# Performance work log

Measured on AMD Instinct MI355X. Metric: run time of the kernel, lower is better.

The kernel has to match this reference:

```python
import jax, jax.numpy as jnp
import numpy as np

D_MODEL = 1024
N_HEADS = 16
HEAD_DIM = D_MODEL // N_HEADS  # 64
SEQ = 2048
BATCH = 2


def setup_inputs() -> dict:
    key = jax.random.key(0)
    ks = jax.random.split(key, 12)
    s = 1.0 / np.sqrt(D_MODEL)
    return {
        "query": jax.random.normal(ks[0], (SEQ, BATCH, D_MODEL), jnp.float32),
        "key": jax.random.normal(ks[1], (SEQ, BATCH, D_MODEL), jnp.float32),
        "value": jax.random.normal(ks[2], (SEQ, BATCH, D_MODEL), jnp.float32),
        "Wq": jax.random.normal(ks[3], (D_MODEL, D_MODEL), jnp.float32) * s,
        "bq": jax.random.normal(ks[4], (D_MODEL,), jnp.float32) * s,
        "Wk": jax.random.normal(ks[5], (D_MODEL, D_MODEL), jnp.float32) * s,
        "bk": jax.random.normal(ks[6], (D_MODEL,), jnp.float32) * s,
        "Wv": jax.random.normal(ks[7], (D_MODEL, D_MODEL), jnp.float32) * s,
        "bv": jax.random.normal(ks[8], (D_MODEL,), jnp.float32) * s,
        "Wo": jax.random.normal(ks[9], (D_MODEL, D_MODEL), jnp.float32) * s,
        "bo": jax.random.normal(ks[10], (D_MODEL,), jnp.float32) * s,
    }


def _rope_tables(seq_len):
    # theta_i = 1 / 10000^(2i/head_dim), i in [0, head_dim//2)
    theta = 1.0 / (10000.0 ** (2.0 * jnp.arange(HEAD_DIM // 2, dtype=jnp.float32) / HEAD_DIM))
    pos = jnp.arange(seq_len, dtype=jnp.float32)[:, None, None, None] * theta  # [S,1,1,hd/2]
    return jnp.sin(pos), jnp.cos(pos)


def _apply_rope(t, sin, cos):
    # t: [S, B, H, hd]; NOTE faithful to source: t2 = q1*sin - q2*cos (minus)
    h = HEAD_DIM // 2
    q1, q2 = t[..., :h], t[..., h:]
    return jnp.concatenate([q1 * cos - q2 * sin, q1 * sin - q2 * cos], axis=-1)


def reference(query, key, value, Wq, bq, Wk, bk, Wv, bv, Wo, bo):
    S, B, _ = query.shape
    q = (query @ Wq.T + bq).reshape(S, B, N_HEADS, HEAD_DIM)
    k = (key @ Wk.T + bk).reshape(S, B, N_HEADS, HEAD_DIM)
    v = (value @ Wv.T + bv).reshape(S, B, N_HEADS, HEAD_DIM)
    sin, cos = _rope_tables(S)
    q = _apply_rope(q, sin, cos)
    k = _apply_rope(k, sin, cos)
    # [S,B,H,d] -> [B,H,S,d]
    q = q.transpose(1, 2, 0, 3)
    k = k.transpose(1, 2, 0, 3)
    v = v.transpose(1, 2, 0, 3)
    scale = 1.0 / jnp.sqrt(jnp.float32(HEAD_DIM))
    scores = jnp.einsum("bhqd,bhkd->bhqk", q, k) * scale
    attn = jax.nn.softmax(scores, axis=-1)
    out = jnp.einsum("bhqk,bhkd->bhqd", attn, v)  # [B,H,S,d]
    out = out.transpose(2, 0, 1, 3).reshape(S, B, D_MODEL)
    return out @ Wo.T + bo
```

## Files before the change

### kernel.cpp

```cpp
#include <hip/hip_runtime.h>
#include <hip/hip_bf16.h>

#define DMODEL 1024
#define NHEADS 16
#define HDIM   64
#define SEQ    2048
#define BATCH  2
#define MROWS  (SEQ*BATCH)

typedef unsigned int u32;
typedef unsigned short u16;
typedef __attribute__((ext_vector_type(8))) short bfrag;
typedef __attribute__((ext_vector_type(4))) float f32x4;
typedef __attribute__((ext_vector_type(16))) float f32x16;
typedef union { u32 u[4]; bfrag f; } fragu;

#define LOG2E 1.44269504088896341f

__device__ __forceinline__ u32 f2bf(float x) {
    unsigned u = __float_as_uint(x);
    return (u + 0x7fffu + ((u >> 16) & 1u)) >> 16;
}
__device__ __forceinline__ float bf2f(u32 h) {
    return __uint_as_float(h << 16);
}
__device__ __forceinline__ u32 pk2bf(float a, float b) {
    __hip_bfloat162 t = __float22bfloat162_rn(make_float2(a, b));
    u32 r;
    __builtin_memcpy(&r, &t, 4);
    return r;
}
__device__ __forceinline__ float fexp2(float x) {
#if __has_builtin(__builtin_amdgcn_exp2f)
    return __builtin_amdgcn_exp2f(x);
#else
    return exp2f(x);
#endif
}
__device__ __forceinline__ u32 pkhi(u32 u0, u32 u1) {
#if __has_builtin(__builtin_amdgcn_perm)
    return __builtin_amdgcn_perm(u1, u0, 0x07060302u);
#else
    return (u0 >> 16) | (u1 & 0xffff0000u);
#endif
}

__device__ __forceinline__ void gld16(const void* g, void* l) {
    __builtin_amdgcn_global_load_lds(
        (const __attribute__((address_space(1))) unsigned int*)g,
        (__attribute__((address_space(3))) unsigned int*)l, 16, 0, 0);
}


__global__ __launch_bounds__(256) void prep_kernel(
    const float* __restrict__ Wq, const float* __restrict__ Wk,
    const float* __restrict__ Wv, const float* __restrict__ Wo,
    u16* __restrict__ wqb, u16* __restrict__ wkb, u16* __restrict__ wvb,
    u16* __restrict__ wob, float2* __restrict__ tab)
{
    const int y = blockIdx.y;
    if (y == 3) {
        if (blockIdx.x >= 256) return;
        const int e = blockIdx.x * 256 + threadIdx.x;
        const int s = e >> 5, i = e & 31;
        const double th = exp(-(double)i * (9.210340371976184 / 32.0));
        double sn, cs;
        sincos((double)s * th, &sn, &cs);
        tab[e] = make_float2((float)sn, (float)cs);
        return;
    }
    const float* src = (y == 0) ? Wq : (y == 1) ? Wk : (y == 2) ? Wv : Wo;
    u16* dst = (y == 0) ? wqb : (y == 1) ? wkb : (y == 2) ? wvb : wob;
    const int lane = threadIdx.x & 63;
    const int wv   = threadIdx.x >> 6;
    const int g8   = lane >> 3;
    const int l8   = lane & 7;
    for (int r = 0; r < 2; ++r) {
        const size_t kb = (size_t)blockIdx.x * 8 + (size_t)r * 4 + wv;
        const float4 x4 = *(const float4*)(src + kb * 256 + lane * 4);
        __align__(8) u16 hb[4];
        __align__(8) u16 lb[4];
        const float xs[4] = {x4.x, x4.y, x4.z, x4.w};
        #pragma unroll
        for (int i = 0; i < 4; ++i) {
            const u32 h = f2bf(xs[i]);
            hb[i] = (u16)h;
            lb[i] = (u16)f2bf(xs[i] - bf2f(h));
        }
        u16* o = dst + kb * 512 + g8 * 64 + l8 * 4;
        *(uint2*)o        = *(const uint2*)hb;
        *(uint2*)(o + 32) = *(const uint2*)lb;
    }
}

__global__ __launch_bounds__(256) void qkv_gemm_kernel(
    const float* __restrict__ query, const float* __restrict__ key,
    const float* __restrict__ value,
    const u16* __restrict__ Wqb, const u16* __restrict__ Wkb,
    const u16* __restrict__ Wvb,
    const float* __restrict__ bq, const float* __restrict__ bk,
    const float* __restrict__ bv, const float2* __restrict__ tab,
    u16* __restrict__ Qh, u16* __restrict__ Ql,
    u16* __restrict__ Kh, u16* __restrict__ Kl,
    u16* __restrict__ VTh)
{
    __shared__ u16 smem16[32768];
    u16* sA = smem16;
    u16* sB = smem16 + 16384;

    const int z  = blockIdx.z;
    const float* Af   = (z == 0) ? query : (z == 1) ? key : value;
    const u16* Wb     = (z == 0) ? Wqb : (z == 1) ? Wkb : Wvb;
    const float* bias = (z == 0) ? bq : (z == 1) ? bk : bv;
    u16* Oh = (z == 0) ? Qh : (z == 1) ? Kh : VTh;
    u16* Ol = (z == 0) ? Ql : (z == 1) ? Kl : nullptr;
    const float rope_scale = (z == 0) ? 0.125f * LOG2E : 1.0f;
    const int mode = (z == 2) ? 1 : 0;

    const int tid   = threadIdx.x;
    const int w     = tid >> 6;
    const int lane  = tid & 63;
    const int lrow  = lane & 15;
    const int lquad = lane >> 4;

    const int id   = blockIdx.x + 16 * blockIdx.y;
    const int xcd  = id & 7;
    const int jj   = id >> 3;
    const int nblk = jj & 7;
    const int mblk = (xcd << 2) | (jj >> 3);
    const int n0   = nblk * 128;
    const int m0   = mblk * 128;

    const int srow8 = lane >> 3;
    const int sch   = (lane & 7) ^ srow8;

    const int l8r = lane >> 3;
    const int l8c = lane & 7;
    const int cA  = l8c >> 1;
    const int hA  = (l8c & 1) * 4;

    int aoffh[2], aoffl[2], boffh[8], boffl[8];
    #pragma unroll
    for (int mi = 0; mi < 2; ++mi) {
        const int ra = w * 32 + mi * 16 + lrow;
        aoffh[mi] = ra * 64 + ((lquad ^ (ra & 7)) << 3);
        aoffl[mi] = ra * 64 + (((lquad + 4) ^ (ra & 7)) << 3);
    }
    #pragma unroll
    for (int ni = 0; ni < 8; ++ni) {
        const int rb = ni * 16 + lrow;
        boffh[ni] = rb * 64 + ((lquad ^ (rb & 7)) << 3);
        boffl[ni] = rb * 64 + (((lquad + 4) ^ (rb & 7)) << 3);
    }

    f32x4 acc[2][8] = {};

    auto stageB = [&](int t) {
        const int h = t & 1;
        #pragma unroll
        for (int i = 0; i < 4; ++i) {
            const int slab = w * 4 + i;
            const int row  = slab * 8 + srow8;
            gld16(Wb + (size_t)(n0 + row) * 2048 + t * 64 + sch * 8,
                  sB + h * 8192 + slab * 512);
        }
    };
    auto loadA = [&](int t, float4* va) {
        #pragma unroll
        for (int i = 0; i < 4; ++i) {
            const int r = w * 32 + i * 8 + l8r;
            va[i] = ((const float4*)Af)[(size_t)(m0 + r) * 256 + t * 8 + l8c];
        }
    };
    auto writeA = [&](int t, const float4* va) {
        const int h = t & 1;
        #pragma unroll
        for (int i = 0; i < 4; ++i) {
            const int r = w * 32 + i * 8 + l8r;
            const u32 u0 = __float_as_uint(va[i].x);
            const u32 u1 = __float_as_uint(va[i].y);
            const u32 u2 = __float_as_uint(va[i].z);
            const u32 u3 = __float_as_uint(va[i].w);
            uint2 hv, lv;
            hv.x = pkhi(u0, u1);
            hv.y = pkhi(u2, u3);
            const float r0 = va[i].x - __uint_as_float(u0 & 0xffff0000u);
            const float r1 = va[i].y - __uint_as_float(u1 & 0xffff0000u);
            const float r2 = va[i].z - __uint_as_float(u2 & 0xffff0000u);
            const float r3 = va[i].w - __uint_as_float(u3 & 0xffff0000u);
            lv.x = pk2bf(r0, r1);
            lv.y = pk2bf(r2, r3);
            u16* base = sA + h * 8192 + r * 64;
            *(uint2*)(base + ((cA ^ (r & 7)) << 3) + hA)       = hv;
            *(uint2*)(base + (((cA + 4) ^ (r & 7)) << 3) + hA) = lv;
        }
    };

    {
        float4 va[4];
        stageB(0);
        loadA(0, va);
        writeA(0, va);
    }
    for (int t = 0; t < 32; ++t) {
        __syncthreads();
        float4 va[4];
        if (t < 31) {
            stageB(t + 1);
            loadA(t + 1, va);
        }
        const int h = t & 1;
        const u16* sAh_ = sA + h * 8192;
        const u16* sBh_ = sB + h * 8192;

        bfrag ah[2], al[2], bh[8], bl[8];
        #pragma unroll
        for (int mi = 0; mi < 2; ++mi) {
            ah[mi] = *(const bfrag*)&sAh_[aoffh[mi]];
            al[mi] = *(const bfrag*)&sAh_[aoffl[mi]];
        }
        #pragma unroll
        for (int ni = 0; ni < 8; ++ni) {
            bh[ni] = *(const bfrag*)&sBh_[boffh[ni]];
            bl[ni] = *(const bfrag*)&sBh_[boffl[ni]];
        }

        #pragma unroll
        for (int mi = 0; mi < 2; ++mi)
            #pragma unroll
            for (int ni = 0; ni < 8; ++ni) {
                acc[mi][ni] = __builtin_amdgcn_mfma_f32_16x16x32_bf16(ah[mi], bh[ni], acc[mi][ni], 0, 0, 0);
                acc[mi][ni] = __builtin_amdgcn_mfma_f32_16x16x32_bf16(ah[mi], bl[ni], acc[mi][ni], 0, 0, 0);
                acc[mi][ni] = __builtin_amdgcn_mfma_f32_16x16x32_bf16(al[mi], bh[ni], acc[mi][ni], 0, 0, 0);
            }

        if (t < 31) writeA(t + 1, va);
    }

    float bn[8];
    #pragma unroll
    for (int ni = 0; ni < 8; ++ni) bn[ni] = bias[n0 + ni * 16 + lrow];

    if (mode == 0) {
        #pragma unroll
        for (int mi = 0; mi < 2; ++mi)
            #pragma unroll
            for (int r = 0; r < 4; ++r) {
                const int mrow = w * 32 + mi * 16 + lquad * 4 + r;
                const int m  = m0 + mrow;
                const int bb = m & 1;
                const int sg = m >> 1;
                #pragma unroll
                for (int hh = 0; hh < 2; ++hh) {
                    const int head = nblk * 2 + hh;
                    const size_t ob = (((size_t)(bb * NHEADS + head) * SEQ) + sg) * HDIM;
                    #pragma unroll
                    for (int ni = 0; ni < 2; ++ni) {
                        const int i = ni * 16 + lrow;
                        const float2 sc = tab[(size_t)sg * 32 + i];
                        const float x1 = acc[mi][hh * 4 + ni][r]     + bn[hh * 4 + ni];
                        const float x2 = acc[mi][hh * 4 + ni + 2][r] + bn[hh * 4 + ni + 2];
                        const float o1 = (x1 * sc.y - x2 * sc.x) * rope_scale;
                        const float o2 = (x1 * sc.x - x2 * sc.y) * rope_scale;
                        const u32 h1 = f2bf(o1);
                        const u32 h2 = f2bf(o2);
                        Oh[ob + i]      = (u16)h1;  Ol[ob + i]      = (u16)f2bf(o1 - bf2f(h1));
                        Oh[ob + i + 32] = (u16)h2;  Ol[ob + i + 32] = (u16)f2bf(o2 - bf2f(h2));
                    }
                }
            }
        return;
    }
    __syncthreads();
    u32* vb = (u32*)smem16;
    for (int p = 0; p < 2; ++p) {
        if (p) __syncthreads();
        #pragma unroll
        for (int mi = 0; mi < 2; ++mi)
            #pragma unroll
            for (int r = 0; r < 4; ++r) {
                const int mrow = w * 32 + mi * 16 + lquad * 4 + r;
                const int bb = mrow & 1;
                const int sl = mrow >> 1;
                if (bb == p) {
                    #pragma unroll
                    for (int ni = 0; ni < 8; ++ni) {
                        const int d = ni * 16 + lrow;
                        vb[d * 65 + sl] = f2bf(acc[mi][ni][r] + bn[ni]);
                    }
                }
            }
        __syncthreads();
        #pragma unroll
        for (int rep = 0; rep < 4; ++rep) {
            const int c  = rep * 256 + tid;
            const int dc = c >> 3;
            const int s8 = c & 7;
            __align__(8) u16 hb[8];
            #pragma unroll
            for (int j = 0; j < 8; ++j)
                hb[j] = (u16)vb[dc * 65 + s8 * 8 + j];
            const int head = nblk * 2 + (dc >> 6);
            const int dd   = dc & 63;
            const size_t orow = ((size_t)(p * NHEADS + head) * HDIM + dd) * SEQ + (m0 >> 1);
            const int blk16 = (s8 >> 1) * 16;
            const int off   = (s8 & 1) * 4;
            *(uint2*)&Oh[orow + blk16 + off]     = *(const uint2*)&hb[0];
            *(uint2*)&Oh[orow + blk16 + 8 + off] = *(const uint2*)&hb[4];
        }
    }
}

template <int NI>
__device__ __forceinline__ void gemm_body(
    int id,
    const u16* __restrict__ Ab, const u16* __restrict__ Wb,
    const float* __restrict__ bias, float* __restrict__ Of,
    u16* smem16)
{
    u16* sA = smem16;
    u16* sB = smem16 + 16384;

    const int tid   = threadIdx.x;
    const int w     = tid >> 6;
    const int lane  = tid & 63;
    const int lrow  = lane & 15;
    const int lquad = lane >> 4;

    const int NBLK = 1024 / (NI * 16);
    const int xcd  = id & 7;
    const int jj   = id >> 3;
    const int nblk = jj & (NBLK - 1);
    const int mblk = (xcd << 2) | (jj / NBLK);
    const int n0   = nblk * NI * 16;
    const int m0   = mblk * 128;

    const int srow8 = lane >> 3;
    const int sch   = (lane & 7) ^ srow8;

    int aoffh[2], aoffl[2], boffh[NI], boffl[NI];
    #pragma unroll
    for (int mi = 0; mi < 2; ++mi) {
        const int ra = w * 32 + mi * 16 + lrow;
        aoffh[mi] = ra * 64 + ((lquad ^ (ra & 7)) << 3);
        aoffl[mi] = ra * 64 + (((lquad + 4) ^ (ra & 7)) << 3);
    }
    #pragma unroll
    for (int ni = 0; ni < NI; ++ni) {
        const int rb = ni * 16 + lrow;
        boffh[ni] = rb * 64 + ((lquad ^ (rb & 7)) << 3);
        boffl[ni] = rb * 64 + (((lquad + 4) ^ (rb & 7)) << 3);
    }

    f32x4 acc[2][NI] = {};

    auto stage = [&](int t) {
        const int h = t & 1;
        #pragma unroll
        for (int i = 0; i < 4; ++i) {
            const int slab = w * 4 + i;
            const int row  = slab * 8 + srow8;
            gld16(Ab + (size_t)(m0 + row) * 2048 + t * 64 + sch * 8,
                  sA + h * 8192 + slab * 512);
        }
        #pragma unroll
        for (int i = 0; i < NI / 2; ++i) {
            const int slab = w * (NI / 2) + i;
            const int row  = slab * 8 + srow8;
            gld16(Wb + (size_t)(n0 + row) * 2048 + t * 64 + sch * 8,
                  sB + h * (NI * 1024) + slab * 512);
        }
    };

    stage(0);
    for (int t = 0; t < 32; ++t) {
        __syncthreads();
        if (t < 31) stage(t + 1);
        const int h = t & 1;
        const u16* sAh_ = sA + h * 8192;
        const u16* sBh_ = sB + h * (NI * 1024);

        bfrag ah[2], al[2], bh[NI], bl[NI];
        #pragma unroll
        for (int mi = 0; mi < 2; ++mi) {
            ah[mi] = *(const bfrag*)&sAh_[aoffh[mi]];
            al[mi] = *(const bfrag*)&sAh_[aoffl[mi]];
        }
        #pragma unroll
        for (int ni = 0; ni < NI; ++ni) {
            bh[ni] = *(const bfrag*)&sBh_[boffh[ni]];
            bl[ni] = *(const bfrag*)&sBh_[boffl[ni]];
        }

        #pragma unroll
        for (int mi = 0; mi < 2; ++mi)
            #pragma unroll
            for (int ni = 0; ni < NI; ++ni) {
                acc[mi][ni] = __builtin_amdgcn_mfma_f32_16x16x32_bf16(ah[mi], bh[ni], acc[mi][ni], 0, 0, 0);
                acc[mi][ni] = __builtin_amdgcn_mfma_f32_16x16x32_bf16(ah[mi], bl[ni], acc[mi][ni], 0, 0, 0);
                acc[mi][ni] = __builtin_amdgcn_mfma_f32_16x16x32_bf16(al[mi], bh[ni], acc[mi][ni], 0, 0, 0);
            }
    }

    float bn[NI];
    #pragma unroll
    for (int ni = 0; ni < NI; ++ni) bn[ni] = bias[n0 + ni * 16 + lrow];

    #pragma unroll
    for (int mi = 0; mi < 2; ++mi)
        #pragma unroll
        for (int r = 0; r < 4; ++r) {
            const int m = m0 + w * 32 + mi * 16 + lquad * 4 + r;
            #pragma unroll
            for (int ni = 0; ni < NI; ++ni)
                Of[(size_t)m * 1024 + n0 + ni * 16 + lrow] = acc[mi][ni][r] + bn[ni];
        }
}

__global__ __launch_bounds__(256) void out_gemm_kernel(
    const u16* __restrict__ Ab, const u16* __restrict__ Wb,
    const float* __restrict__ bias, float* __restrict__ Of)
{
    __shared__ u16 smem16[24576];
    const int id = blockIdx.x + 16 * blockIdx.y;
    gemm_body<4>(id, Ab, Wb, bias, Of, smem16);
}

__global__ __launch_bounds__(256) void attn_mfma_kernel(
    const u16* __restrict__ Qh, const u16* __restrict__ Ql,
    const u16* __restrict__ Kh, const u16* __restrict__ Kl,
    const u16* __restrict__ Vh,
    u16* __restrict__ AOb)
{
    __shared__ u16 sKh[8192], sKl[8192];
    __shared__ u16 sVh[8192];

    const int tid  = threadIdx.x;
    const int w    = tid >> 6;
    const int lane = tid & 63;
    const int l31  = lane & 31;
    const int g    = lane >> 5;

    const int id = blockIdx.x + 16 * blockIdx.y;
    const int jj = id >> 3;
    const int bh = ((id & 7) << 2) | (jj >> 4);
    const int qt = jj & 15;

    const size_t qg = ((size_t)bh * SEQ + qt * 128 + w * 32 + l31) * HDIM + g * 8;
    bfrag qfh[4], qfl[4];
    #pragma unroll
    for (int ks = 0; ks < 4; ++ks) {
        qfh[ks] = *(const bfrag*)&Qh[qg + ks * 16];
        qfl[ks] = *(const bfrag*)&Ql[qg + ks * 16];
    }

    const int srow   = lane >> 3;
    const int schunk = (lane & 7) ^ srow;
    const u16* gsrc = nullptr; u16* lbase = nullptr; size_t istep = 0, ktstep = 0;
    if (w == 0) {
        gsrc = Kh + ((size_t)bh * SEQ + srow) * HDIM + schunk * 8;
        istep = 8 * 64; ktstep = 64 * 64; lbase = sKh;
    } else if (w == 1) {
        gsrc = Kl + ((size_t)bh * SEQ + srow) * HDIM + schunk * 8;
        istep = 8 * 64; ktstep = 64 * 64; lbase = sKl;
    } else if (w == 2) {
        gsrc = Vh + ((size_t)bh * HDIM + srow) * SEQ + schunk * 8;
        istep = 8 * SEQ; ktstep = 64; lbase = sVh;
    }

    int koff[2][4];
    #pragma unroll
    for (int a = 0; a < 2; ++a) {
        const int row = a * 32 + l31;
        #pragma unroll
        for (int c = 0; c < 4; ++c)
            koff[a][c] = row * 64 + (((c * 2 + g) ^ (row & 7)) << 3);
    }

    f32x16 accO[2] = {};
    float l_loc = 0.0f;

    auto stage = [&](int kt) {
        if (w < 3) {
            const u16* gp = gsrc + (size_t)kt * ktstep;
            u16* dst = lbase + (kt & 1) * 4096;
            #pragma unroll
            for (int i = 0; i < 8; ++i)
                gld16(gp + (size_t)i * istep, dst + i * 512);
        }
    };

    stage(0);
    for (int kt = 0; kt < SEQ / 64; ++kt) {
        __syncthreads();
        if (kt < SEQ / 64 - 1) stage(kt + 1);
        const int po = (kt & 1) * 4096;

        f32x16 accS[2] = {};
        #pragma unroll
        for (int kg = 0; kg < 2; ++kg)
            #pragma unroll
            for (int ks = 0; ks < 4; ++ks) {
                const bfrag kh_ = *(const bfrag*)&sKh[po + koff[kg][ks]];
                const bfrag kl_ = *(const bfrag*)&sKl[po + koff[kg][ks]];
                accS[kg] = __builtin_amdgcn_mfma_f32_32x32x16_bf16(kh_, qfh[ks], accS[kg], 0, 0, 0);
                accS[kg] = __builtin_amdgcn_mfma_f32_32x32x16_bf16(kh_, qfl[ks], accS[kg], 0, 0, 0);
                accS[kg] = __builtin_amdgcn_mfma_f32_32x32x16_bf16(kl_, qfh[ks], accS[kg], 0, 0, 0);
            }

        float pv[2][16];
        #pragma unroll
        for (int kg = 0; kg < 2; ++kg)
            #pragma unroll
            for (int r = 0; r < 16; ++r) {
                const float p = fexp2(accS[kg][r]);
                pv[kg][r] = p;
                l_loc += p;
            }

        #pragma unroll
        for (int kp = 0; kp < 4; ++kp) {
            const int kg = kp >> 1;
            const int t8 = (kp & 1) * 8;
            fragu ph;
            #pragma unroll
            for (int j2 = 0; j2 < 4; ++j2)
                ph.u[j2] = pk2bf(pv[kg][t8 + 2 * j2], pv[kg][t8 + 2 * j2 + 1]);
            #pragma unroll
            for (int dt = 0; dt < 2; ++dt) {
                const bfrag vh = *(const bfrag*)&sVh[po + koff[dt][kp]];
                accO[dt] = __builtin_amdgcn_mfma_f32_32x32x16_bf16(vh, ph.f, accO[dt], 0, 0, 0);
            }
        }
    }

    const float inv = 1.0f / (l_loc + __shfl_xor(l_loc, 32));

    const int b = bh >> 4;
    const int h = bh & 15;
    const int sg = qt * 128 + w * 32 + l31;
    const int rm = sg * BATCH + b;
    #pragma unroll
    for (int dt = 0; dt < 2; ++dt)
        #pragma unroll
        for (int rq = 0; rq < 4; ++rq) {
            const int j0 = 8 * rq + 4 * g;
            const int t  = h * 2 + dt;
            __align__(8) u16 hb[4];
            __align__(8) u16 lb[4];
            #pragma unroll
            for (int i2 = 0; i2 < 4; ++i2) {
                const float v = accO[dt][rq * 4 + i2] * inv;
                const u32 hh = f2bf(v);
                hb[i2] = (u16)hh;
                lb[i2] = (u16)f2bf(v - bf2f(hh));
            }
            u16* o = AOb + (size_t)rm * 2048 + t * 64 + j0;
            *(uint2*)o        = *(const uint2*)hb;
            *(uint2*)(o + 32) = *(const uint2*)lb;
        }
}

extern "C" void kernel_launch(void* const* d_in, const int* in_sizes, int n_in,
                              void* d_out, int out_size, void* d_ws, size_t ws_size,
                              hipStream_t stream)
{
    const float* query = (const float*)d_in[0];
    const float* key   = (const float*)d_in[1];
    const float* value = (const float*)d_in[2];
    const float* Wq    = (const float*)d_in[3];
    const float* bq    = (const float*)d_in[4];
    const float* Wk    = (const float*)d_in[5];
    const float* bk    = (const float*)d_in[6];
    const float* Wv    = (const float*)d_in[7];
    const float* bv    = (const float*)d_in[8];
    const float* Wo    = (const float*)d_in[9];
    const float* bo    = (const float*)d_in[10];
    float* out = (float*)d_out;

    char* wsb = (char*)d_ws;
    const size_t MB = 1024 * 1024;
    u16* Wqb = (u16*)(wsb + 0 * MB);
    u16* Wkb = (u16*)(wsb + 4 * MB);
    u16* Wvb = (u16*)(wsb + 8 * MB);
    float2* tab = (float2*)(wsb + 12 * MB);
    u16* Qh  = (u16*)(wsb + 16 * MB); u16* Ql  = (u16*)(wsb + 24 * MB);
    u16* Kh  = (u16*)(wsb + 32 * MB); u16* Kl  = (u16*)(wsb + 40 * MB);
    u16* VTh = (u16*)(wsb + 48 * MB);
    u16* Wob = (u16*)(wsb + 56 * MB);
    u16* AOb = (u16*)(wsb + 0 * MB);

    prep_kernel<<<dim3(512, 5), 256, 0, stream>>>(
        Wq, Wk, Wv, Wo, Wqb, Wkb, Wvb, Wob, tab);
    qkv_gemm_kernel<<<dim3(16, 16, 3), 256, 0, stream>>>(
        query, key, value,
        Wqb, Wkb, Wvb, bq, bk, bv, tab, Qh, Ql, Kh, Kl, VTh);
    attn_mfma_kernel<<<dim3(16, 32), 256, 0, stream>>>(
        Qh, Ql, Kh, Kl, VTh, AOb);
    out_gemm_kernel<<<dim3(16, 32), 256, 0, stream>>>(AOb, Wob, bo, out);
}
```

Baseline: 316.0 us.

## Stage fp32 A tiles via direct global-to-LDS loads and split to bf16 after LDS read

```diff
diff --git a/kernel.cpp b/kernel.cpp
--- a/kernel.cpp
+++ b/kernel.cpp
@@ -105,8 +105,8 @@
     u16* __restrict__ VTh)
 {
     __shared__ u16 smem16[32768];
-    u16* sA = smem16;
-    u16* sB = smem16 + 16384;
+    float* sAf = (float*)smem16;
+    u16*   sB  = smem16 + 16384;
 
     const int z  = blockIdx.z;
     const float* Af   = (z == 0) ? query : (z == 1) ? key : value;
@@ -134,18 +134,14 @@
     const int srow8 = lane >> 3;
     const int sch   = (lane & 7) ^ srow8;
 
-    const int l8r = lane >> 3;
-    const int l8c = lane & 7;
-    const int cA  = l8c >> 1;
-    const int hA  = (l8c & 1) * 4;
-
-    int aoffh[2], aoffl[2], boffh[8], boffl[8];
+    int aoff0[2], aoff1[2];
     #pragma unroll
     for (int mi = 0; mi < 2; ++mi) {
         const int ra = w * 32 + mi * 16 + lrow;
-        aoffh[mi] = ra * 64 + ((lquad ^ (ra & 7)) << 3);
-        aoffl[mi] = ra * 64 + (((lquad + 4) ^ (ra & 7)) << 3);
-    }
+        aoff0[mi] = ra * 32 + (((2 * lquad)     ^ (ra & 7)) << 2);
+        aoff1[mi] = ra * 32 + (((2 * lquad + 1) ^ (ra & 7)) << 2);
+    }
+    int boffh[8], boffl[8];
     #pragma unroll
     for (int ni = 0; ni < 8; ++ni) {
         const int rb = ni * 16 + lrow;
@@ -155,69 +151,52 @@
 
     f32x4 acc[2][8] = {};
 
-    auto stageB = [&](int t) {
+    auto stage = [&](int t) {
         const int h = t & 1;
         #pragma unroll
         for (int i = 0; i < 4; ++i) {
             const int slab = w * 4 + i;
             const int row  = slab * 8 + srow8;
+            gld16(Af + (size_t)(m0 + row) * 1024 + t * 32 + sch * 4,
+                  sAf + h * 4096 + slab * 256);
             gld16(Wb + (size_t)(n0 + row) * 2048 + t * 64 + sch * 8,
                   sB + h * 8192 + slab * 512);
         }
     };
-    auto loadA = [&](int t, float4* va) {
-        #pragma unroll
-        for (int i = 0; i < 4; ++i) {
-            const int r = w * 32 + i * 8 + l8r;
-            va[i] = ((const float4*)Af)[(size_t)(m0 + r) * 256 + t * 8 + l8c];
-        }
+
+    auto cvtAB = [&](const f32x4 a, const f32x4 b, bfrag& hi8, bfrag& lo8) {
+        const u32 u0 = __float_as_uint(a[0]), u1 = __float_as_uint(a[1]);
+        const u32 u2 = __float_as_uint(a[2]), u3 = __float_as_uint(a[3]);
+        const u32 u4 = __float_as_uint(b[0]), u5 = __float_as_uint(b[1]);
+        const u32 u6 = __float_as_uint(b[2]), u7 = __float_as_uint(b[3]);
+        fragu fh, fl;
+        fh.u[0] = pkhi(u0, u1); fh.u[1] = pkhi(u2, u3);
+        fh.u[2] = pkhi(u4, u5); fh.u[3] = pkhi(u6, u7);
+        fl.u[0] = pk2bf(a[0] - __uint_as_float(u0 & 0xffff0000u),
+                        a[1] - __uint_as_float(u1 & 0xffff0000u));
+        fl.u[1] = pk2bf(a[2] - __uint_as_float(u2 & 0xffff0000u),
+                        a[3] - __uint_as_float(u3 & 0xffff0000u));
+        fl.u[2] = pk2bf(b[0] - __uint_as_float(u4 & 0xffff0000u),
+                        b[1] - __uint_as_float(u5 & 0xffff0000u));
+        fl.u[3] = pk2bf(b[2] - __uint_as_float(u6 & 0xffff0000u),
+                        b[3] - __uint_as_float(u7 & 0xffff0000u));
+        hi8 = fh.f; lo8 = fl.f;
     };
-    auto writeA = [&](int t, const float4* va) {
-        const int h = t & 1;
-        #pragma unroll
-        for (int i = 0; i < 4; ++i) {
-            const int r = w * 32 + i * 8 + l8r;
-            const u32 u0 = __float_as_uint(va[i].x);
-            const u32 u1 = __float_as_uint(va[i].y);
-            const u32 u2 = __float_as_uint(va[i].z);
-            const u32 u3 = __float_as_uint(va[i].w);
-            uint2 hv, lv;
-            hv.x = pkhi(u0, u1);
-            hv.y = pkhi(u2, u3);
-            const float r0 = va[i].x - __uint_as_float(u0 & 0xffff0000u);
-            const float r1 = va[i].y - __uint_as_float(u1 & 0xffff0000u);
-            const float r2 = va[i].z - __uint_as_float(u2 & 0xffff0000u);
-            const float r3 = va[i].w - __uint_as_float(u3 & 0xffff0000u);
-            lv.x = pk2bf(r0, r1);
-            lv.y = pk2bf(r2, r3);
-            u16* base = sA + h * 8192 + r * 64;
-            *(uint2*)(base + ((cA ^ (r & 7)) << 3) + hA)       = hv;
-            *(uint2*)(base + (((cA + 4) ^ (r & 7)) << 3) + hA) = lv;
-        }
-    };
-
-    {
-        float4 va[4];
-        stageB(0);
-        loadA(0, va);
-        writeA(0, va);
-    }
+
+    stage(0);
     for (int t = 0; t < 32; ++t) {
         __syncthreads();
-        float4 va[4];
-        if (t < 31) {
-            stageB(t + 1);
-            loadA(t + 1, va);
-        }
+        if (t < 31) stage(t + 1);
         const int h = t & 1;
-        const u16* sAh_ = sA + h * 8192;
-        const u16* sBh_ = sB + h * 8192;
+        const float* sAh_ = sAf + h * 4096;
+        const u16*   sBh_ = sB + h * 8192;
 
         bfrag ah[2], al[2], bh[8], bl[8];
         #pragma unroll
         for (int mi = 0; mi < 2; ++mi) {
-            ah[mi] = *(const bfrag*)&sAh_[aoffh[mi]];
-            al[mi] = *(const bfrag*)&sAh_[aoffl[mi]];
+            const f32x4 a0 = *(const f32x4*)&sAh_[aoff0[mi]];
+            const f32x4 a1 = *(const f32x4*)&sAh_[aoff1[mi]];
+            cvtAB(a0, a1, ah[mi], al[mi]);
         }
         #pragma unroll
         for (int ni = 0; ni < 8; ++ni) {
@@ -233,8 +212,6 @@
                 acc[mi][ni] = __builtin_amdgcn_mfma_f32_16x16x32_bf16(ah[mi], bl[ni], acc[mi][ni], 0, 0, 0);
                 acc[mi][ni] = __builtin_amdgcn_mfma_f32_16x16x32_bf16(al[mi], bh[ni], acc[mi][ni], 0, 0, 0);
             }
-
-        if (t < 31) writeA(t + 1, va);
     }
 
     float bn[8];
```

Result: faster. 295.8 us (-6.4%).
